# Kernel tuning notes

Measured on AMD Instinct MI355X. Metric: run time of the kernel, lower is better.

Reference implementation:

```python
import jax, jax.numpy as jnp
import numpy as np

B, L, H, IN = 64, 2048, 512, 1


def setup_inputs() -> dict:
    key = jax.random.key(0)
    ks = jax.random.split(key, 7)
    s = 1.0 / np.sqrt(H)  # torch GRUCell init: U(-1/sqrt(H), 1/sqrt(H))
    x = jax.random.normal(ks[0], (B, L, IN), dtype=jnp.float32)
    state = jax.random.normal(ks[1], (B, H), dtype=jnp.float32)
    W_ih = jax.random.uniform(ks[2], (3 * H, IN), minval=-s, maxval=s, dtype=jnp.float32)
    W_hh = jax.random.uniform(ks[3], (3 * H, H), minval=-s, maxval=s, dtype=jnp.float32)
    b_ih = jax.random.uniform(ks[4], (3 * H,), minval=-s, maxval=s, dtype=jnp.float32)
    b_hh = jax.random.uniform(ks[5], (3 * H,), minval=-s, maxval=s, dtype=jnp.float32)
    A = jnp.array([0.001], dtype=jnp.float32)
    return {"x": x, "state": state, "W_ih": W_ih, "W_hh": W_hh,
            "b_ih": b_ih, "b_hh": b_hh, "A": A}


def reference(x, state, W_ih, W_hh, b_ih, b_hh, A):
    # Precompute input projections for all timesteps: [B, L, 3H] -> [L, B, 3H]
    gi = jnp.einsum('bli,gi->blg', x, W_ih) + b_ih
    gi = jnp.swapaxes(gi, 0, 1)

    def step(carry, gi_t):
        residual, st = carry
        gh = residual @ W_hh.T + b_hh            # [B, 3H]
        i_r, i_z, i_n = jnp.split(gi_t, 3, axis=-1)
        h_r, h_z, h_n = jnp.split(gh, 3, axis=-1)
        r = jax.nn.sigmoid(i_r + h_r)
        z = jax.nn.sigmoid(i_z + h_z)
        n = jnp.tanh(i_n + r * h_n)
        residual = (1.0 - z) * n + z * residual  # GRUCell output
        st = st + A * residual                   # scaled residual accumulation
        return (residual, st), st

    # residual initialized to state.clone(); accumulator starts at state
    (_, final_state), outs = jax.lax.scan(step, (state, state), gi)
    out = jnp.swapaxes(outs, 0, 1)               # [B, L, H]
    return out, final_state
```

## Files before the change

### kernel.cpp

```cpp
#include <hip/hip_runtime.h>
#include <math.h>


#define BB_ 64
#define LL_ 2048
#define HH_ 512
#define NGROUP 8
#define GBLK 32
#define BGRP 8
#define HBLK 16
#define NT 512
#define RROW (HH_ + 4)

#define FLAG_STRIDE 32
#define FLAG_BYTES (NGROUP * GBLK * FLAG_STRIDE * 4)

typedef float f32x2 __attribute__((ext_vector_type(2)));
typedef float f32x4 __attribute__((ext_vector_type(4)));

template<int CTRL>
__device__ __forceinline__ float dpp_add(float x) {
    int s = __builtin_amdgcn_update_dpp(0, __float_as_int(x), CTRL, 0xF, 0xF, true);
    return x + __int_as_float(s);
}

__device__ __forceinline__ f32x4 load_f4_coherent(const float* p) {
    f32x4 r;
    asm volatile("global_load_dwordx4 %0, %1, off sc0 sc1" : "=v"(r) : "v"(p) : "memory");
    return r;
}
__device__ __forceinline__ void store_f4_coherent(float* p, f32x4 v) {
    asm volatile("global_store_dwordx4 %0, %1, off sc0 sc1" : : "v"(p), "v"(v) : "memory");
}
__device__ __forceinline__ void store_dw_coherent(unsigned* p, unsigned v) {
    asm volatile("global_store_dword %0, %1, off sc0 sc1" : : "v"(p), "v"(v) : "memory");
}
__device__ __forceinline__ void vm0() {
    asm volatile("s_waitcnt vmcnt(0)" ::: "memory");
    __builtin_amdgcn_sched_barrier(0);
}
__device__ __forceinline__ void pkfma(f32x2& acc, f32x2 a, f32x2 b) {
    asm("v_pk_fma_f32 %0, %1, %2, %0" : "+v"(acc) : "v"(a), "v"(b));
}

__global__ __launch_bounds__(NT, 2)
void gru_scan_kernel(const float* __restrict__ x,
                     const float* __restrict__ state,
                     const float* __restrict__ W_ih,
                     const float* __restrict__ W_hh,
                     const float* __restrict__ b_ih,
                     const float* __restrict__ b_hh,
                     const float* __restrict__ A,
                     float* __restrict__ out,
                     char* __restrict__ ws) {
    __shared__ float W_s[48][HH_];
    __shared__ __align__(16) float res_s[BGRP][RROW];
    __shared__ float x_s[BGRP][128];
    __shared__ float wih_s[48], bih_s[48], bhh_s[48];
    __shared__ __align__(16) float res_out_s[BGRP][HBLK];
    __shared__ __align__(16) float out_s[BGRP][HBLK];

    const int tid = threadIdx.x;
    const int bid = blockIdx.x;
    const int g   = bid >> 5;
    const int j   = bid & 31;
    const int b0  = g * BGRP;
    const int h0  = j * HBLK;

    const int w    = tid >> 6;
    const int lane = tid & 63;
    const int bg   = lane >> 4;
    const int ksub = lane & 15;

    unsigned* flags = (unsigned*)ws;
    unsigned* grp_flags = flags + (size_t)g * GBLK * FLAG_STRIDE;
    float* resA = (float*)(ws + FLAG_BYTES);
    float* resB = resA + BB_ * HH_;

    #pragma unroll
    for (int gg = 0; gg < 3; ++gg)
        for (int i = tid; i < HBLK * HH_; i += NT) {
            int hl = i >> 9, k = i & 511;
            W_s[gg * 16 + hl][k] = W_hh[(size_t)(gg * HH_ + h0 + hl) * HH_ + k];
        }
    for (int i = tid; i < 48; i += NT) {
        int gg = i >> 4, hl = i & 15;
        int row = gg * HH_ + h0 + hl;
        wih_s[i] = W_ih[row];
        bih_s[i] = b_ih[row];
        bhh_s[i] = b_hh[row];
    }
    const float Aval = A[0];

    float st[2][2];
    #pragma unroll
    for (int bl = 0; bl < 2; ++bl)
        #pragma unroll
        for (int hh = 0; hh < 2; ++hh)
            st[bl][hh] = state[(size_t)(b0 + 2 * bg + bl) * HH_ + h0 + 2 * w + hh];

    const f32x2* W2 = (const f32x2*)&W_s[0][0];
    const f32x2* R2 = (const f32x2*)&res_s[0][0];

    for (int t = 0; t < LL_; ++t) {
        if ((t & 127) == 0) {
            for (int i = tid; i < BGRP * 128; i += NT) {
                int bb = i >> 7, kk = i & 127;
                x_s[bb][kk] = x[(size_t)(b0 + bb) * LL_ + t + kk];
            }
        }
        {
            const int c0 = tid, c1 = tid + NT;
            const int b_0 = c0 >> 7, q0 = c0 & 127;
            const int b_1 = c1 >> 7, q1 = c1 & 127;
            f32x4 v0, v1;
            if (t == 0) {
                v0 = *(const f32x4*)&state[(size_t)(b0 + b_0) * HH_ + q0 * 4];
                v1 = *(const f32x4*)&state[(size_t)(b0 + b_1) * HH_ + q1 * 4];
            } else {
                const float* rbuf = (t & 1) ? resB : resA;
                v0 = load_f4_coherent(&rbuf[(size_t)(b0 + b_0) * HH_ + q0 * 4]);
                v1 = load_f4_coherent(&rbuf[(size_t)(b0 + b_1) * HH_ + q1 * 4]);
                vm0();
            }
            *(f32x4*)&res_s[b_0][q0 * 4] = v0;
            *(f32x4*)&res_s[b_1][q1 * 4] = v1;
        }
        __syncthreads();

        f32x2 rv2[2][16];
        #pragma unroll
        for (int bl = 0; bl < 2; ++bl) {
            const int rowb = (2 * bg + bl) * (RROW / 2);
            #pragma unroll
            for (int m = 0; m < 8; ++m) {
                rv2[bl][2 * m]     = R2[rowb + (m * 16 + ksub) * 2];
                rv2[bl][2 * m + 1] = R2[rowb + (m * 16 + ksub) * 2 + 1];
            }
        }

        f32x2 acc2[6][2];
        #pragma unroll
        for (int rr = 0; rr < 6; ++rr) {
            acc2[rr][0] = (f32x2){0.f, 0.f};
            acc2[rr][1] = (f32x2){0.f, 0.f};
        }
        #pragma unroll
        for (int rr = 0; rr < 6; ++rr) {
            const int gg = rr >> 1, hh = rr & 1;
            const int lr = gg * 16 + 2 * w + hh;
            #pragma unroll
            for (int m = 0; m < 8; ++m) {
                f32x2 w0 = W2[lr * 256 + (m * 16 + ksub) * 2];
                f32x2 w1 = W2[lr * 256 + (m * 16 + ksub) * 2 + 1];
                #pragma unroll
                for (int bl = 0; bl < 2; ++bl) {
                    pkfma(acc2[rr][bl], w0, rv2[bl][2 * m]);
                    pkfma(acc2[rr][bl], w1, rv2[bl][2 * m + 1]);
                }
            }
        }

        float acc[6][2];
        #pragma unroll
        for (int rr = 0; rr < 6; ++rr)
            #pragma unroll
            for (int bl = 0; bl < 2; ++bl) {
                float v = acc2[rr][bl].x + acc2[rr][bl].y;
                v = dpp_add<0x111>(v);
                v = dpp_add<0x112>(v);
                v = dpp_add<0x114>(v);
                v = dpp_add<0x118>(v);
                acc[rr][bl] = v;
            }

        if (ksub == 15) {
            #pragma unroll
            for (int bl = 0; bl < 2; ++bl) {
                const int b = 2 * bg + bl;
                const float xv = x_s[b][t & 127];
                #pragma unroll
                for (int hh = 0; hh < 2; ++hh) {
                    const int hl = 2 * w + hh;
                    float hr = acc[hh][bl]     + bhh_s[hl];
                    float hz = acc[2 + hh][bl] + bhh_s[16 + hl];
                    float hn = acc[4 + hh][bl] + bhh_s[32 + hl];
                    float ir = xv * wih_s[hl]      + bih_s[hl];
                    float iz = xv * wih_s[16 + hl] + bih_s[16 + hl];
                    float in_ = xv * wih_s[32 + hl] + bih_s[32 + hl];
                    float r = 1.f / (1.f + __expf(-(ir + hr)));
                    float z = 1.f / (1.f + __expf(-(iz + hz)));
                    float n = tanhf(in_ + r * hn);
                    float oldr = res_s[b][h0 + hl];
                    float nr = (1.f - z) * n + z * oldr;
                    st[bl][hh] += Aval * nr;
                    res_out_s[b][hl] = nr;
                    out_s[b][hl] = st[bl][hh];
                }
            }
        }
        __syncthreads();

        if (w == 0) {
            float* wbuf = (t & 1) ? resA : resB;
            const unsigned target = (unsigned)(t + 1);
            if (lane < 32) {
                const int b = lane >> 2, p = lane & 3;
                store_f4_coherent(&wbuf[(size_t)(b0 + b) * HH_ + h0 + p * 4],
                                  *(f32x4*)&res_out_s[b][p * 4]);
            }
            vm0();
            if (lane == 0)
                store_dw_coherent(&grp_flags[j * FLAG_STRIDE], target);
            if (lane < 32) {
                const int b = lane >> 2, p = lane & 3;
                *(f32x4*)&out[((size_t)(b0 + b) * LL_ + t) * HH_ + h0 + p * 4] =
                    *(f32x4*)&out_s[b][p * 4];
            }
            unsigned v;
            do {
                v = (lane < GBLK)
                    ? __hip_atomic_load(&grp_flags[lane * FLAG_STRIDE],
                                        __ATOMIC_RELAXED, __HIP_MEMORY_SCOPE_AGENT)
                    : target;
            } while (!__all((int)(v >= target)));
        }
        __syncthreads();
    }

    if (ksub == 15) {
        #pragma unroll
        for (int bl = 0; bl < 2; ++bl)
            #pragma unroll
            for (int hh = 0; hh < 2; ++hh) {
                const int bglob = b0 + 2 * bg + bl;
                const int hglob = h0 + 2 * w + hh;
                out[(size_t)BB_ * LL_ * HH_ + (size_t)bglob * HH_ + hglob] = st[bl][hh];
            }
    }
}

extern "C" void kernel_launch(void* const* d_in, const int* in_sizes, int n_in,
                              void* d_out, int out_size, void* d_ws, size_t ws_size,
                              hipStream_t stream) {
    (void)in_sizes; (void)n_in; (void)out_size; (void)ws_size;
    const float* x     = (const float*)d_in[0];
    const float* state = (const float*)d_in[1];
    const float* W_ih  = (const float*)d_in[2];
    const float* W_hh  = (const float*)d_in[3];
    const float* b_ih  = (const float*)d_in[4];
    const float* b_hh  = (const float*)d_in[5];
    const float* A     = (const float*)d_in[6];

    hipMemsetAsync(d_ws, 0, FLAG_BYTES, stream);
    hipLaunchKernelGGL(gru_scan_kernel, dim3(NGROUP * GBLK), dim3(NT), 0, stream,
                       x, state, W_ih, W_hh, b_ih, b_hh, A,
                       (float*)d_out, (char*)d_ws);
}
```

Baseline: 10.22 ms.

## Split hidden dimension across 64 blocks per group with 8 rows each

Doubles the number of cooperating blocks per batch group (512 blocks total) so each block handles 8 hidden units instead of 16. Per-step matvec work and register pressure per block roughly halve, and occupancy is raised to 4 blocks per CU. The change also packs flags more densely, adds s_sleep to the spin-wait and uses 128-bit LDS reads. In exchange, the per-step barrier now has to wait on 64 flags instead of 32, which adds synchronisation latency.

Result: slower. 10.65 ms (+4.1%).

```diff
diff --git a/kernel.cpp b/kernel.cpp
--- a/kernel.cpp
+++ b/kernel.cpp
@@ -6,13 +6,14 @@
 #define LL_ 2048
 #define HH_ 512
 #define NGROUP 8
-#define GBLK 32
+#define GBLK 64
 #define BGRP 8
-#define HBLK 16
+#define HBLK 8
 #define NT 512
-#define RROW (HH_ + 4)
-
-#define FLAG_STRIDE 32
+#define RROW 516
+#define XROW 132
+
+#define FLAG_STRIDE 4
 #define FLAG_BYTES (NGROUP * GBLK * FLAG_STRIDE * 4)
 
 typedef float f32x2 __attribute__((ext_vector_type(2)));
@@ -43,7 +44,7 @@
     asm("v_pk_fma_f32 %0, %1, %2, %0" : "+v"(acc) : "v"(a), "v"(b));
 }
 
-__global__ __launch_bounds__(NT, 2)
+__global__ __launch_bounds__(NT, 4)
 void gru_scan_kernel(const float* __restrict__ x,
                      const float* __restrict__ state,
                      const float* __restrict__ W_ih,
@@ -53,17 +54,17 @@
                      const float* __restrict__ A,
                      float* __restrict__ out,
                      char* __restrict__ ws) {
-    __shared__ float W_s[48][HH_];
+    __shared__ float W_s[24][HH_];
     __shared__ __align__(16) float res_s[BGRP][RROW];
-    __shared__ float x_s[BGRP][128];
-    __shared__ float wih_s[48], bih_s[48], bhh_s[48];
+    __shared__ float x_s[BGRP][XROW];
+    __shared__ float wih_s[24], bih_s[24], bhh_s[24];
     __shared__ __align__(16) float res_out_s[BGRP][HBLK];
     __shared__ __align__(16) float out_s[BGRP][HBLK];
 
     const int tid = threadIdx.x;
     const int bid = blockIdx.x;
-    const int g   = bid >> 5;
-    const int j   = bid & 31;
+    const int g   = bid >> 6;
+    const int j   = bid & 63;
     const int b0  = g * BGRP;
     const int h0  = j * HBLK;
 
@@ -77,30 +78,27 @@
     float* resA = (float*)(ws + FLAG_BYTES);
     float* resB = resA + BB_ * HH_;
 
-    #pragma unroll
-    for (int gg = 0; gg < 3; ++gg)
-        for (int i = tid; i < HBLK * HH_; i += NT) {
-            int hl = i >> 9, k = i & 511;
-            W_s[gg * 16 + hl][k] = W_hh[(size_t)(gg * HH_ + h0 + hl) * HH_ + k];
-        }
-    for (int i = tid; i < 48; i += NT) {
-        int gg = i >> 4, hl = i & 15;
-        int row = gg * HH_ + h0 + hl;
-        wih_s[i] = W_ih[row];
-        bih_s[i] = b_ih[row];
-        bhh_s[i] = b_hh[row];
+    for (int i = tid; i < 24 * HH_; i += NT) {
+        int row = i >> 9, k = i & 511;
+        int gate = row >> 3, hl = row & 7;
+        W_s[row][k] = W_hh[(size_t)(gate * HH_ + h0 + hl) * HH_ + k];
+    }
+    if (tid < 24) {
+        int gate = tid >> 3, hl = tid & 7;
+        int row = gate * HH_ + h0 + hl;
+        wih_s[tid] = W_ih[row];
+        bih_s[tid] = b_ih[row];
+        bhh_s[tid] = b_hh[row];
     }
     const float Aval = A[0];
 
-    float st[2][2];
+    float st[2];
     #pragma unroll
     for (int bl = 0; bl < 2; ++bl)
-        #pragma unroll
-        for (int hh = 0; hh < 2; ++hh)
-            st[bl][hh] = state[(size_t)(b0 + 2 * bg + bl) * HH_ + h0 + 2 * w + hh];
-
-    const f32x2* W2 = (const f32x2*)&W_s[0][0];
-    const f32x2* R2 = (const f32x2*)&res_s[0][0];
+        st[bl] = state[(size_t)(b0 + 2 * bg + bl) * HH_ + h0 + w];
+
+    const f32x4* W4 = (const f32x4*)&W_s[0][0];
+    const f32x4* R4 = (const f32x4*)&res_s[0][0];
 
     for (int t = 0; t < LL_; ++t) {
         if ((t & 127) == 0) {
@@ -128,50 +126,51 @@
         }
         __syncthreads();
 
-        f32x2 rv2[2][16];
+        f32x4 rv4[2][8];
         #pragma unroll
         for (int bl = 0; bl < 2; ++bl) {
-            const int rowb = (2 * bg + bl) * (RROW / 2);
+            const int rowb = (2 * bg + bl) * (RROW / 4);
+            #pragma unroll
+            for (int m = 0; m < 8; ++m)
+                rv4[bl][m] = R4[rowb + m * 16 + ksub];
+        }
+
+        f32x2 acc2[3][2];
+        #pragma unroll
+        for (int gate = 0; gate < 3; ++gate) {
+            acc2[gate][0] = (f32x2){0.f, 0.f};
+            acc2[gate][1] = (f32x2){0.f, 0.f};
+        }
+        #pragma unroll
+        for (int gate = 0; gate < 3; ++gate) {
+            const int lr = gate * 8 + w;
             #pragma unroll
             for (int m = 0; m < 8; ++m) {
-                rv2[bl][2 * m]     = R2[rowb + (m * 16 + ksub) * 2];
-                rv2[bl][2 * m + 1] = R2[rowb + (m * 16 + ksub) * 2 + 1];
-            }
-        }
-
-        f32x2 acc2[6][2];
-        #pragma unroll
-        for (int rr = 0; rr < 6; ++rr) {
-            acc2[rr][0] = (f32x2){0.f, 0.f};
-            acc2[rr][1] = (f32x2){0.f, 0.f};
-        }
-        #pragma unroll
-        for (int rr = 0; rr < 6; ++rr) {
-            const int gg = rr >> 1, hh = rr & 1;
-            const int lr = gg * 16 + 2 * w + hh;
-            #pragma unroll
-            for (int m = 0; m < 8; ++m) {
-                f32x2 w0 = W2[lr * 256 + (m * 16 + ksub) * 2];
-                f32x2 w1 = W2[lr * 256 + (m * 16 + ksub) * 2 + 1];
+                f32x4 wv = W4[lr * 128 + m * 16 + ksub];
+                f32x2 wlo = __builtin_shufflevector(wv, wv, 0, 1);
+                f32x2 whi = __builtin_shufflevector(wv, wv, 2, 3);
                 #pragma unroll
                 for (int bl = 0; bl < 2; ++bl) {
-                    pkfma(acc2[rr][bl], w0, rv2[bl][2 * m]);
-                    pkfma(acc2[rr][bl], w1, rv2[bl][2 * m + 1]);
+                    f32x4 rv = rv4[bl][m];
+                    f32x2 rlo = __builtin_shufflevector(rv, rv, 0, 1);
+                    f32x2 rhi = __builtin_shufflevector(rv, rv, 2, 3);
+                    pkfma(acc2[gate][bl], wlo, rlo);
+                    pkfma(acc2[gate][bl], whi, rhi);
                 }
             }
         }
 
-        float acc[6][2];
-        #pragma unroll
-        for (int rr = 0; rr < 6; ++rr)
+        float acc[3][2];
+        #pragma unroll
+        for (int gate = 0; gate < 3; ++gate)
             #pragma unroll
             for (int bl = 0; bl < 2; ++bl) {
-                float v = acc2[rr][bl].x + acc2[rr][bl].y;
+                float v = acc2[gate][bl].x + acc2[gate][bl].y;
                 v = dpp_add<0x111>(v);
                 v = dpp_add<0x112>(v);
                 v = dpp_add<0x114>(v);
                 v = dpp_add<0x118>(v);
-                acc[rr][bl] = v;
+                acc[gate][bl] = v;
             }
 
         if (ksub == 15) {
@@ -179,24 +178,20 @@
             for (int bl = 0; bl < 2; ++bl) {
                 const int b = 2 * bg + bl;
                 const float xv = x_s[b][t & 127];
-                #pragma unroll
-                for (int hh = 0; hh < 2; ++hh) {
-                    const int hl = 2 * w + hh;
-                    float hr = acc[hh][bl]     + bhh_s[hl];
-                    float hz = acc[2 + hh][bl] + bhh_s[16 + hl];
-                    float hn = acc[4 + hh][bl] + bhh_s[32 + hl];
-                    float ir = xv * wih_s[hl]      + bih_s[hl];
-                    float iz = xv * wih_s[16 + hl] + bih_s[16 + hl];
-                    float in_ = xv * wih_s[32 + hl] + bih_s[32 + hl];
-                    float r = 1.f / (1.f + __expf(-(ir + hr)));
-                    float z = 1.f / (1.f + __expf(-(iz + hz)));
-                    float n = tanhf(in_ + r * hn);
-                    float oldr = res_s[b][h0 + hl];
-                    float nr = (1.f - z) * n + z * oldr;
-                    st[bl][hh] += Aval * nr;
-                    res_out_s[b][hl] = nr;
-                    out_s[b][hl] = st[bl][hh];
-                }
+                float hr = acc[0][bl] + bhh_s[w];
+                float hz = acc[1][bl] + bhh_s[8 + w];
+                float hn = acc[2][bl] + bhh_s[16 + w];
+                float ir = xv * wih_s[w]      + bih_s[w];
+                float iz = xv * wih_s[8 + w]  + bih_s[8 + w];
+                float in_ = xv * wih_s[16 + w] + bih_s[16 + w];
+                float r = 1.f / (1.f + __expf(-(ir + hr)));
+                float z = 1.f / (1.f + __expf(-(iz + hz)));
+                float n = tanhf(in_ + r * hn);
+                float oldr = res_s[b][h0 + w];
+                float nr = (1.f - z) * n + z * oldr;
+                st[bl] += Aval * nr;
+                res_out_s[b][w] = nr;
+                out_s[b][w] = st[bl];
             }
         }
         __syncthreads();
@@ -204,25 +199,24 @@
         if (w == 0) {
             float* wbuf = (t & 1) ? resA : resB;
             const unsigned target = (unsigned)(t + 1);
-            if (lane < 32) {
-                const int b = lane >> 2, p = lane & 3;
+            if (lane < 16) {
+                const int b = lane >> 1, p = lane & 1;
                 store_f4_coherent(&wbuf[(size_t)(b0 + b) * HH_ + h0 + p * 4],
                                   *(f32x4*)&res_out_s[b][p * 4]);
             }
             vm0();
             if (lane == 0)
                 store_dw_coherent(&grp_flags[j * FLAG_STRIDE], target);
-            if (lane < 32) {
-                const int b = lane >> 2, p = lane & 3;
+            if (lane < 16) {
+                const int b = lane >> 1, p = lane & 1;
                 *(f32x4*)&out[((size_t)(b0 + b) * LL_ + t) * HH_ + h0 + p * 4] =
                     *(f32x4*)&out_s[b][p * 4];
             }
             unsigned v;
             do {
-                v = (lane < GBLK)
-                    ? __hip_atomic_load(&grp_flags[lane * FLAG_STRIDE],
-                                        __ATOMIC_RELAXED, __HIP_MEMORY_SCOPE_AGENT)
-                    : target;
+                __builtin_amdgcn_s_sleep(1);
+                v = __hip_atomic_load(&grp_flags[lane * FLAG_STRIDE],
+                                      __ATOMIC_RELAXED, __HIP_MEMORY_SCOPE_AGENT);
             } while (!__all((int)(v >= target)));
         }
         __syncthreads();
@@ -230,13 +224,10 @@
 
     if (ksub == 15) {
         #pragma unroll
-        for (int bl = 0; bl < 2; ++bl)
-            #pragma unroll
-            for (int hh = 0; hh < 2; ++hh) {
-                const int bglob = b0 + 2 * bg + bl;
-                const int hglob = h0 + 2 * w + hh;
-                out[(size_t)BB_ * LL_ * HH_ + (size_t)bglob * HH_ + hglob] = st[bl][hh];
-            }
+        for (int bl = 0; bl < 2; ++bl) {
+            const int bglob = b0 + 2 * bg + bl;
+            out[(size_t)BB_ * LL_ * HH_ + (size_t)bglob * HH_ + h0 + w] = st[bl];
+        }
     }
 }
 
```
